# Kernel tuning notes

Hardware: AMD Instinct MI355X
Metric: run time of the kernel (lower is better)

The kernel has to match this reference:

```python
import jax, jax.numpy as jnp
import numpy as np

B, L, N, C = 16, 96, 1024, 3
EMB, GRAP, OUT, NLAYER = 64, 16, 12, 2


def setup_inputs() -> dict:
    key = jax.random.key(0)
    ks = jax.random.split(key, 16)
    s = 0.1
    return {
        "history_data": jax.random.normal(ks[0], (B, L, N, C), jnp.float32),
        # row-stochastic graph (normalized adjacency buffer)
        "adj": jax.nn.softmax(jax.random.normal(ks[1], (N, N), jnp.float32), axis=-1),
        "Wv0": jax.random.normal(ks[2], (C, EMB), jnp.float32) * s,
        "Wv1": jax.random.normal(ks[3], (EMB, EMB), jnp.float32) * s,
        "bv": jnp.zeros((NLAYER, EMB), jnp.float32),
        "E": jax.random.normal(ks[4], (NLAYER, N, EMB), jnp.float32) * s,
        "Wq": jax.random.normal(ks[5], (NLAYER, EMB, EMB), jnp.float32) * s,
        "Wk": jax.random.normal(ks[6], (NLAYER, EMB, EMB), jnp.float32) * s,
        "Eg1": jax.random.normal(ks[7], (NLAYER, N, GRAP), jnp.float32) * s,
        "Eg2": jax.random.normal(ks[8], (NLAYER, N, GRAP), jnp.float32) * s,
        "Wmix": jax.random.normal(ks[9], (NLAYER, 3, EMB, EMB), jnp.float32) * s,
        "bmix": jnp.zeros((NLAYER, EMB), jnp.float32),
        "Wgates": jax.random.normal(ks[10], (NLAYER, 4, EMB, EMB), jnp.float32) * s,
        "bgates": jnp.zeros((NLAYER, 4, EMB), jnp.float32),
        "Wdec": jax.random.normal(ks[11], (OUT, NLAYER, EMB), jnp.float32) * s,
        "bdec": jnp.zeros((OUT,), jnp.float32),
        "Wout": jax.random.normal(ks[12], (OUT, OUT), jnp.float32) * s,
        "bout": jnp.zeros((OUT,), jnp.float32),
    }


def reference(history_data, adj, Wv0, Wv1, bv, E, Wq, Wk, Eg1, Eg2,
              Wmix, bmix, Wgates, bgates, Wdec, bdec, Wout, bout):
    # GinAR forward (inference: dropout = identity, lay_norm unused in original forward).
    emb = Wv1.shape[0]
    inv = 1.0 / jnp.sqrt(jnp.float32(emb))
    x = history_data  # (B, L, N, in)
    finals = []
    for z in range(Wmix.shape[0]):
        Wv = Wv0 if z == 0 else Wv1
        # interpolation attention over variables (nodes), shared across time/batch
        q = E[z] @ Wq[z]
        k = E[z] @ Wk[z]
        attn = jax.nn.softmax((q @ k.T) * inv, axis=-1)                 # (N, N)
        # adaptive learned graph
        adp = jax.nn.softmax(jax.nn.relu(Eg1[z] @ Eg2[z].T), axis=-1)    # (N, N)
        bz, Wm, bm, Wg, bgz = bv[z], Wmix[z], bmix[z], Wgates[z], bgates[z]

        def step(ct, xt, Wv=Wv, attn=attn, adp=adp, bz=bz, Wm=Wm, bm=bm, Wg=Wg, bgz=bgz):
            v = xt @ Wv + bz                                # (B, N, emb)
            h = jnp.einsum('mn,bne->bme', attn, v)          # variable interpolation
            hg = (jnp.einsum('mn,bne->bme', adj, h) @ Wm[0]
                  + jnp.einsum('mn,bne->bme', adp, h) @ Wm[1]
                  + h @ Wm[2] + bm)                         # adaptive graph conv
            gates = jnp.einsum('bne,kef->kbnf', hg, Wg) + bgz[:, None, None, :]
            f = jax.nn.sigmoid(gates[0])
            i = jax.nn.sigmoid(gates[1])
            g = jnp.tanh(gates[2])
            o = jax.nn.sigmoid(gates[3])
            ct = f * ct + i * g
            ht = o * jnp.tanh(ct)
            return ct, ht

        ct0 = jnp.zeros((x.shape[0], x.shape[2], emb), x.dtype)
        _, hts = jax.lax.scan(step, ct0, jnp.moveaxis(x, 1, 0))  # (L, B, N, emb)
        x = jnp.moveaxis(hts, 0, 1)                              # (B, L, N, emb)
        finals.append(x[:, -1])                                  # last step -> (B, N, emb)
    final = jnp.stack(finals, axis=1)                            # (B, layers, N, emb)
    # decoder Conv2d(layer_num -> out_len, kernel (1, emb)) == contraction over (layer, emb)
    dec = jnp.einsum('blne,ole->bon', final, Wdec) + bdec[None, :, None]
    # 1x1 output conv
    out = jnp.einsum('bpn,op->bon', dec, Wout) + bout[None, :, None]
    return out  # (B, out_len, N)
```

## Files before the change

kernel.cpp:

```cpp
#include <hip/hip_runtime.h>
#include <hip/hip_bf16.h>

#define B_ 16
#define L_ 96
#define N_ 1024
#define EMB_ 64

typedef __hip_bfloat16 bf16;
typedef __attribute__((ext_vector_type(4))) float f32x4;
typedef __attribute__((ext_vector_type(8))) short s16x8;

__global__ __launch_bounds__(256) void gemm_nn(
    const float* __restrict__ A, const float* __restrict__ Bm, float* __restrict__ C,
    int M, int N, int K, int lda, int ldb, int ldc, const float* __restrict__ bias)
{
    __shared__ float As[64][17];
    __shared__ __align__(16) float Bs[16][64];
    const int tid = threadIdx.x;
    const int tx = tid & 15, ty = tid >> 4;
    const int row0 = blockIdx.y * 64, col0 = blockIdx.x * 64;
    float acc[4][4] = {};
    const int ak = tid & 15, ar = tid >> 4;
    const int bc = tid & 63, bk = tid >> 6;
    for (int k0 = 0; k0 < K; k0 += 16) {
#pragma unroll
        for (int i = 0; i < 4; ++i) {
            int r = ar + i * 16;
            int gr = row0 + r, gk = k0 + ak;
            As[r][ak] = (gr < M && gk < K) ? A[(size_t)gr * lda + gk] : 0.f;
        }
#pragma unroll
        for (int i = 0; i < 4; ++i) {
            int kk = bk + i * 4;
            int gk = k0 + kk, gc = col0 + bc;
            Bs[kk][bc] = (gk < K && gc < N) ? Bm[(size_t)gk * ldb + gc] : 0.f;
        }
        __syncthreads();
#pragma unroll
        for (int kk = 0; kk < 16; ++kk) {
            float4 b4 = *reinterpret_cast<const float4*>(&Bs[kk][tx * 4]);
            float a0 = As[ty * 4 + 0][kk];
            float a1 = As[ty * 4 + 1][kk];
            float a2 = As[ty * 4 + 2][kk];
            float a3 = As[ty * 4 + 3][kk];
            acc[0][0] += a0 * b4.x; acc[0][1] += a0 * b4.y; acc[0][2] += a0 * b4.z; acc[0][3] += a0 * b4.w;
            acc[1][0] += a1 * b4.x; acc[1][1] += a1 * b4.y; acc[1][2] += a1 * b4.z; acc[1][3] += a1 * b4.w;
            acc[2][0] += a2 * b4.x; acc[2][1] += a2 * b4.y; acc[2][2] += a2 * b4.z; acc[2][3] += a2 * b4.w;
            acc[3][0] += a3 * b4.x; acc[3][1] += a3 * b4.y; acc[3][2] += a3 * b4.z; acc[3][3] += a3 * b4.w;
        }
        __syncthreads();
    }
#pragma unroll
    for (int i = 0; i < 4; ++i) {
        int gr = row0 + ty * 4 + i;
        if (gr >= M) continue;
#pragma unroll
        for (int j = 0; j < 4; ++j) {
            int gc = col0 + tx * 4 + j;
            if (gc >= N) continue;
            float v = acc[i][j];
            if (bias) v += bias[gc];
            C[(size_t)gr * ldc + gc] = v;
        }
    }
}

__global__ __launch_bounds__(256) void gemm_nt(
    const float* __restrict__ A, const float* __restrict__ Bm, float* __restrict__ C,
    int N, int K, float alpha)
{
    __shared__ float As[64][65];
    __shared__ float Bs[64][65];
    const int tid = threadIdx.x;
    const int row0 = blockIdx.y * 64, col0 = blockIdx.x * 64;
    for (int idx = tid; idx < 64 * K; idx += 256) {
        int r = idx / K, c = idx % K;
        As[r][c] = A[(size_t)(row0 + r) * K + c];
        Bs[r][c] = Bm[(size_t)(col0 + r) * K + c];
    }
    __syncthreads();
    const int tx = tid & 15, ty = tid >> 4;
    float acc[4][4] = {};
    for (int c = 0; c < K; ++c) {
        float a[4], b[4];
#pragma unroll
        for (int i = 0; i < 4; ++i) a[i] = As[ty * 4 + i][c];
#pragma unroll
        for (int j = 0; j < 4; ++j) b[j] = Bs[tx * 4 + j][c];
#pragma unroll
        for (int i = 0; i < 4; ++i)
#pragma unroll
            for (int j = 0; j < 4; ++j) acc[i][j] += a[i] * b[j];
    }
#pragma unroll
    for (int i = 0; i < 4; ++i)
#pragma unroll
        for (int j = 0; j < 4; ++j)
            C[(size_t)(row0 + ty * 4 + i) * N + col0 + tx * 4 + j] = alpha * acc[i][j];
}

__global__ __launch_bounds__(256) void row_softmax(
    const float* __restrict__ in, float* __restrict__ out32, int os32,
    bf16* __restrict__ out16, int os16, int relu)
{
    const float* rp = in + (size_t)blockIdx.x * N_;
    const int tid = threadIdx.x;
    float v[4];
#pragma unroll
    for (int j = 0; j < 4; ++j) {
        float x = rp[tid + 256 * j];
        if (relu) x = fmaxf(x, 0.f);
        v[j] = x;
    }
    float m = fmaxf(fmaxf(v[0], v[1]), fmaxf(v[2], v[3]));
#pragma unroll
    for (int off = 32; off > 0; off >>= 1) m = fmaxf(m, __shfl_xor(m, off));
    __shared__ float red[4], red2[4];
    int w = tid >> 6;
    if ((tid & 63) == 0) red[w] = m;
    __syncthreads();
    m = fmaxf(fmaxf(red[0], red[1]), fmaxf(red[2], red[3]));
    float s = 0.f;
#pragma unroll
    for (int j = 0; j < 4; ++j) { v[j] = __expf(v[j] - m); s += v[j]; }
#pragma unroll
    for (int off = 32; off > 0; off >>= 1) s += __shfl_xor(s, off);
    if ((tid & 63) == 0) red2[w] = s;
    __syncthreads();
    s = red2[0] + red2[1] + red2[2] + red2[3];
    float inv = 1.f / s;
#pragma unroll
    for (int j = 0; j < 4; ++j) {
        float r = v[j] * inv;
        if (out32) out32[(size_t)blockIdx.x * os32 + tid + 256 * j] = r;
        if (out16) out16[(size_t)blockIdx.x * os16 + tid + 256 * j] = __float2bfloat16(r);
    }
}

__global__ __launch_bounds__(256) void transpose_f2b(
    const float* __restrict__ in, bf16* __restrict__ out)
{
    __shared__ float t[64][65];
    const int cx = blockIdx.x, cy = blockIdx.y;
    const int tid = threadIdx.x;
#pragma unroll
    for (int k = 0; k < 16; ++k) {
        int idx = k * 256 + tid;
        int r = idx >> 6, c = idx & 63;
        t[r][c] = in[(size_t)(cy * 64 + r) * 1024 + cx * 64 + c];
    }
    __syncthreads();
#pragma unroll
    for (int k = 0; k < 16; ++k) {
        int idx = k * 256 + tid;
        int r = idx >> 6, c = idx & 63;
        out[(size_t)(cx * 64 + r) * 1024 + cy * 64 + c] = __float2bfloat16(t[c][r]);
    }
}

__global__ __launch_bounds__(256) void wgct_kernel(const float* __restrict__ Wg,
                                                   bf16* __restrict__ WgcT)
{
    int i = blockIdx.x * 256 + threadIdx.x;
    int g = i >> 12, e = (i >> 6) & 63, f = i & 63;
    WgcT[(((size_t)g * 64 + f) << 6) + e] = __float2bfloat16(Wg[i]);
}

__global__ __launch_bounds__(256) void wvc1t_kernel(const float* __restrict__ Wvc1,
                                                    bf16* __restrict__ WT)
{
    int i = blockIdx.x * 256 + threadIdx.x;
    int row = i >> 6, f = i & 63;
    float v = 0.f;
    if (row < 192) { int kp = row >> 6, e = row & 63; v = Wvc1[kp * 4096 + f * 64 + e]; }
    WT[i] = __float2bfloat16(v);
}

__global__ __launch_bounds__(256) void f2b_kernel(const float* __restrict__ in,
                                                  bf16* __restrict__ out, int n)
{
    int i = blockIdx.x * 256 + threadIdx.x;
    if (i < n) out[i] = __float2bfloat16(in[i]);
}

__global__ __launch_bounds__(256) void bias_kernel(
    const float* __restrict__ bvz, const float* __restrict__ Wmz, const float* __restrict__ bmz,
    const float* __restrict__ Wgz, const float* __restrict__ bgz, float* __restrict__ bgconst)
{
    __shared__ float bconst[64];
    const int tid = threadIdx.x;
    if (tid < 64) {
        float s = bmz[tid];
        for (int kp = 0; kp < 3; ++kp)
            for (int f = 0; f < 64; ++f) s += bvz[f] * Wmz[kp * 4096 + f * 64 + tid];
        bconst[tid] = s;
    }
    __syncthreads();
    int g = tid >> 6, fo = tid & 63;
    float s = bgz[g * 64 + fo];
    for (int e = 0; e < 64; ++e) s += bconst[e] * Wgz[g * 4096 + e * 64 + fo];
    bgconst[tid] = s;
}

__global__ __launch_bounds__(256) void wbig_kernel(
    const float* __restrict__ Wvc0, const float* __restrict__ Wg0, bf16* __restrict__ WbigT)
{
    const int tid = threadIdx.x;
    const int g = tid >> 6, fo = tid & 63;
    float v[9];
#pragma unroll
    for (int q = 0; q < 9; ++q) {
        const int kp = q / 3, c = q % 3;
        float s = 0.f;
        for (int e = 0; e < 64; ++e)
            s += Wvc0[kp * 192 + c * 64 + e] * Wg0[g * 4096 + e * 64 + fo];
        v[q] = s;
    }
#pragma unroll
    for (int i = 0; i < 32; ++i)
        WbigT[(size_t)tid * 32 + i] = __float2bfloat16(i < 9 ? v[i] : 0.f);
}

__global__ __launch_bounds__(256) void xt_build(
    const float* __restrict__ hist, bf16* __restrict__ XT)
{
    __shared__ float xs[3][1024];
    const int lb = blockIdx.x;
    const int l = lb >> 4, b = lb & 15;
    const int tid = threadIdx.x;
    const float* xp = hist + ((size_t)b * L_ + l) * N_ * 3;
    for (int i = tid; i < 3072; i += 256) xs[i % 3][i / 3] = xp[i];
    __syncthreads();
#pragma unroll
    for (int c = 0; c < 3; ++c)
#pragma unroll
        for (int q = 0; q < 4; ++q) {
            int n = q * 256 + tid;
            XT[((size_t)lb * 3 + c) * 1024 + n] = __float2bfloat16(xs[c][n]);
        }
}

__device__ __forceinline__ void gload16(const bf16* g, bf16* l)
{
    __builtin_amdgcn_global_load_lds((const __attribute__((address_space(1))) void*)g,
                                     (__attribute__((address_space(3))) void*)l, 16, 0, 0);
}

template <int OUT_BF16, int REMAP>
__global__ __launch_bounds__(256) void gemm_mfma(
    const bf16* __restrict__ A, const bf16* __restrict__ BT, void* __restrict__ Cp,
    int M, int N, int K, int lda, int ldb, int ldc,
    const float* __restrict__ bias, int Nmask)
{
    __shared__ __align__(16) bf16 As[128 * 64];
    __shared__ __align__(16) bf16 Bs[128 * 64];
    const int tid = threadIdx.x;
    const int lane = tid & 63, w = tid >> 6;
    const int wr = w >> 1, wc = w & 1;
    const int row0 = blockIdx.y * 128, col0 = blockIdx.x * 128;
    if (REMAP == 1) BT += (size_t)blockIdx.z * 64;
    if (REMAP == 2) A += (size_t)blockIdx.z * 1024;
    if (REMAP == 3) {
        const int z3 = blockIdx.z >> 1, wh = blockIdx.z & 1;
        if (wh) A = BT + (size_t)z3 * 1048576;
        BT = (const bf16*)bias + (size_t)z3 * 1048576;
        Cp = (void*)((bf16*)Cp + (size_t)z3 * 3145728 + (size_t)wh * 1024);
        bias = nullptr;
    }

    f32x4 acc[4][4];
#pragma unroll
    for (int i = 0; i < 4; ++i)
#pragma unroll
        for (int j = 0; j < 4; ++j) acc[i][j] = (f32x4){0.f, 0.f, 0.f, 0.f};

    const int srow = w * 32 + (lane >> 3);
    const int scolsw = ((lane & 7) ^ (lane >> 3)) * 8;

    for (int k0 = 0; k0 < K; k0 += 64) {
#pragma unroll
        for (int i = 0; i < 4; ++i) {
            gload16(A + (size_t)(row0 + srow + i * 8) * lda + k0 + scolsw,
                    &As[(w * 32 + i * 8) * 64]);
            gload16(BT + (size_t)(col0 + srow + i * 8) * ldb + k0 + scolsw,
                    &Bs[(w * 32 + i * 8) * 64]);
        }
        __syncthreads();
#pragma unroll
        for (int kk = 0; kk < 64; kk += 32) {
            s16x8 af[4], bfr[4];
            const int ko = (kk + (lane >> 4) * 8) ^ ((lane & 7) << 3);
#pragma unroll
            for (int mi = 0; mi < 4; ++mi)
                af[mi] = *(const s16x8*)&As[(wr * 64 + mi * 16 + (lane & 15)) * 64 + ko];
#pragma unroll
            for (int ni = 0; ni < 4; ++ni)
                bfr[ni] = *(const s16x8*)&Bs[(wc * 64 + ni * 16 + (lane & 15)) * 64 + ko];
#pragma unroll
            for (int mi = 0; mi < 4; ++mi)
#pragma unroll
                for (int ni = 0; ni < 4; ++ni)
                    acc[mi][ni] = __builtin_amdgcn_mfma_f32_16x16x32_bf16(
                        af[mi], bfr[ni], acc[mi][ni], 0, 0, 0);
        }
        __syncthreads();
    }

    if (REMAP == 1) {
        bf16* outb = (bf16*)Cp + (size_t)blockIdx.z * (64 * 3072);
#pragma unroll
        for (int mi = 0; mi < 4; ++mi) {
            const int gr = row0 + wr * 64 + mi * 16 + (lane >> 4) * 4;
#pragma unroll
            for (int ni = 0; ni < 4; ++ni) {
                const int gc = col0 + wc * 64 + ni * 16 + (lane & 15);
#pragma unroll
                for (int j = 0; j < 4; ++j) {
                    const int r = gr + j;
                    if (r >= Nmask) continue;
                    outb[(size_t)(r & 63) * 3072 + (r >> 6) * 1024 + gc] =
                        __float2bfloat16(acc[mi][ni][j]);
                }
            }
        }
        return;
    }
    if (REMAP == 2) {
        bf16* outb = (bf16*)Cp;
        const int kpoff = blockIdx.z * 3;
#pragma unroll
        for (int mi = 0; mi < 4; ++mi) {
            const int gr = row0 + wr * 64 + mi * 16 + (lane >> 4) * 4;
#pragma unroll
            for (int ni = 0; ni < 4; ++ni) {
                const int gc = col0 + wc * 64 + ni * 16 + (lane & 15);
                if (gc >= Nmask) continue;
                const int dstc = (gc / 3) * 32 + kpoff + gc % 3;
#pragma unroll
                for (int j = 0; j < 4; ++j)
                    outb[(size_t)(gr + j) * ldc + dstc] = __float2bfloat16(acc[mi][ni][j]);
            }
        }
        return;
    }

#pragma unroll
    for (int mi = 0; mi < 4; ++mi) {
        const int gr = row0 + wr * 64 + mi * 16 + (lane >> 4) * 4;
#pragma unroll
        for (int ni = 0; ni < 4; ++ni) {
            const int gc = col0 + wc * 64 + ni * 16 + (lane & 15);
            if (gc >= Nmask) continue;
            const float bb = bias ? bias[gc] : 0.f;
#pragma unroll
            for (int j = 0; j < 4; ++j) {
                float v = acc[mi][ni][j] + bb;
                if (OUT_BF16)
                    ((bf16*)Cp)[(size_t)(gr + j) * ldc + gc] = __float2bfloat16(v);
                else
                    ((float*)Cp)[(size_t)(gr + j) * ldc + gc] = v;
            }
        }
    }
}

__global__ __launch_bounds__(512) void gemm_pipe(
    const bf16* __restrict__ A, const bf16* __restrict__ BT, bf16* __restrict__ C,
    int N, int K)
{
    __shared__ __align__(16) bf16 lds[8 * 8192];
    const int tid = threadIdx.x;
    const int lane = tid & 63, w = tid >> 6;
    const int wm = w >> 2, wn = w & 3, bh = wn >> 1;
    const int row0 = blockIdx.y * 256, col0 = blockIdx.x * 256;

    const int strow = tid >> 3;
    const int srck  = ((tid & 7) ^ ((tid >> 3) & 7)) << 3;
    const int e7 = lane & 7, fs = lane >> 4, a15 = lane & 15;

    int aoff0[8], boff0[4];
#pragma unroll
    for (int mi = 0; mi < 8; ++mi)
        aoff0[mi] = (mi * 16 + a15) * 64 + ((fs ^ e7) << 3);
#pragma unroll
    for (int ni = 0; ni < 4; ++ni)
        boff0[ni] = ((wn & 1) * 64 + ni * 16 + a15) * 64 + ((fs ^ e7) << 3);

    auto stage = [&](int mat, int half, int kt) {
        bf16* dst = &lds[(size_t)((((kt & 1) << 1) | mat) * 2 + half) * 8192 + w * 512];
        const bf16* src = (mat ? BT + (size_t)col0 * K : A + (size_t)row0 * K)
                          + (size_t)(half * 128) * K + kt * 64 + srck;
        gload16(src + (size_t)strow * K, dst);
        gload16(src + (size_t)(64 + strow) * K, dst + 4096);
    };

    f32x4 acc[8][4];
#pragma unroll
    for (int i = 0; i < 8; ++i)
#pragma unroll
        for (int j = 0; j < 4; ++j) acc[i][j] = (f32x4){0.f, 0.f, 0.f, 0.f};

    s16x8 b0, b1, b2, b3;

#define MF_(a, mi) { \
    acc[mi][0] = __builtin_amdgcn_mfma_f32_16x16x32_bf16(a, b0, acc[mi][0], 0, 0, 0); \
    acc[mi][1] = __builtin_amdgcn_mfma_f32_16x16x32_bf16(a, b1, acc[mi][1], 0, 0, 0); \
    acc[mi][2] = __builtin_amdgcn_mfma_f32_16x16x32_bf16(a, b2, acc[mi][2], 0, 0, 0); \
    acc[mi][3] = __builtin_amdgcn_mfma_f32_16x16x32_bf16(a, b3, acc[mi][3], 0, 0, 0); }

#define PH_(d, kh, g, DOB, STG) { \
    const bf16* Ab = &lds[((d) * 4 + wm) * 8192]; \
    const bf16* Bb = &lds[((d) * 4 + 2 + bh) * 8192]; \
    if (DOB) { \
        b0 = *(const s16x8*)&Bb[boff0[0] ^ ((kh) * 32)]; \
        b1 = *(const s16x8*)&Bb[boff0[1] ^ ((kh) * 32)]; \
        b2 = *(const s16x8*)&Bb[boff0[2] ^ ((kh) * 32)]; \
        b3 = *(const s16x8*)&Bb[boff0[3] ^ ((kh) * 32)]; \
    } \
    s16x8 a0 = *(const s16x8*)&Ab[aoff0[(g) * 4 + 0] ^ ((kh) * 32)]; \
    s16x8 a1 = *(const s16x8*)&Ab[aoff0[(g) * 4 + 1] ^ ((kh) * 32)]; \
    s16x8 a2 = *(const s16x8*)&Ab[aoff0[(g) * 4 + 2] ^ ((kh) * 32)]; \
    s16x8 a3 = *(const s16x8*)&Ab[aoff0[(g) * 4 + 3] ^ ((kh) * 32)]; \
    STG; \
    __builtin_amdgcn_s_barrier(); \
    asm volatile("s_waitcnt lgkmcnt(0)" ::: "memory"); \
    __builtin_amdgcn_sched_barrier(0); \
    __builtin_amdgcn_s_setprio(1); \
    MF_(a0, (g) * 4 + 0); MF_(a1, (g) * 4 + 1); \
    MF_(a2, (g) * 4 + 2); MF_(a3, (g) * 4 + 3); \
    __builtin_amdgcn_s_setprio(0); \
    __builtin_amdgcn_s_barrier(); }

    const int NT = K >> 6;
    stage(0, 0, 0); stage(0, 1, 0); stage(1, 0, 0); stage(1, 1, 0);
    stage(0, 0, 1);

    for (int i = 0; i < NT / 2; ++i) {
        const int kt = 2 * i;
        asm volatile("s_waitcnt vmcnt(2)" ::: "memory");
        __builtin_amdgcn_sched_barrier(0);
        __builtin_amdgcn_s_barrier();
        PH_(0, 0, 0, 1, { stage(0, 1, kt + 1); });
        PH_(0, 0, 1, 0, { stage(1, 0, kt + 1); });
        PH_(0, 1, 0, 1, { stage(1, 1, kt + 1); });
        PH_(0, 1, 1, 0, { if (kt + 2 < NT) stage(0, 0, kt + 2); });
        if (kt + 2 < NT) { asm volatile("s_waitcnt vmcnt(2)" ::: "memory"); }
        else             { asm volatile("s_waitcnt vmcnt(0)" ::: "memory"); }
        __builtin_amdgcn_sched_barrier(0);
        __builtin_amdgcn_s_barrier();
        PH_(1, 0, 0, 1, { if (kt + 2 < NT) stage(0, 1, kt + 2); });
        PH_(1, 0, 1, 0, { if (kt + 2 < NT) stage(1, 0, kt + 2); });
        PH_(1, 1, 0, 1, { if (kt + 2 < NT) stage(1, 1, kt + 2); });
        PH_(1, 1, 1, 0, { if (kt + 3 < NT) stage(0, 0, kt + 3); });
    }
#undef PH_
#undef MF_

#pragma unroll
    for (int mi = 0; mi < 8; ++mi) {
        const int gr = row0 + wm * 128 + mi * 16 + (lane >> 4) * 4;
#pragma unroll
        for (int ni = 0; ni < 4; ++ni) {
            const int gc = col0 + wn * 64 + ni * 16 + (lane & 15);
#pragma unroll
            for (int j = 0; j < 4; ++j)
                C[(size_t)(gr + j) * N + gc] = __float2bfloat16(acc[mi][ni][j]);
        }
    }
}

__global__ __launch_bounds__(256, 4) void fused_gates_scan(
    const bf16* __restrict__ HG, const bf16* __restrict__ WgcT,
    const float* __restrict__ bgc, float* __restrict__ ct_buf,
    bf16* __restrict__ ht_out, float* __restrict__ htlast,
    int LC, int l0, int initct)
{
    __shared__ __align__(16) bf16 Bs[256 * 64];
    __shared__ float bgs[256];
    const int tid = threadIdx.x;
    const int lane = tid & 63, w = tid >> 6;
    const int n = blockIdx.x;
    const int swz = ((lane & 7) ^ (lane >> 3)) * 8;
    const int l8 = (lane >> 3) * 64;

#pragma unroll
    for (int r = 0; r < 8; ++r)
        gload16(WgcT + r * 2048 + w * 512 + l8 + swz, &Bs[r * 2048 + w * 512]);
    bgs[tid] = bgc[tid];
    __syncthreads();

    const int ar = lane & 15;
    const int ak = (lane >> 4) * 8;
    const int kswz = (lane & 7) << 3;
    const int f = w * 16 + ar;
    const int r0 = (lane >> 4) * 4;
    const float bgf = bgs[f], bgi = bgs[64 + f], bgg = bgs[128 + f], bgo = bgs[192 + f];

    float ct[4];
    const size_t cbase = (size_t)n * 1024;
#pragma unroll
    for (int j = 0; j < 4; ++j)
        ct[j] = initct ? 0.f : ct_buf[cbase + (size_t)(r0 + j) * 64 + f];

    const bf16* HGn = HG + (size_t)n * LC * 1024;
    s16x8 a0 = *(const s16x8*)&HGn[ar * 64 + ak];
    s16x8 a1 = *(const s16x8*)&HGn[ar * 64 + ak + 32];

    for (int l = 0; l < LC; ++l) {
        s16x8 p0 = a0, p1 = a1;
        if (l + 1 < LC) {
            p0 = *(const s16x8*)&HGn[((l + 1) * 16 + ar) * 64 + ak];
            p1 = *(const s16x8*)&HGn[((l + 1) * 16 + ar) * 64 + ak + 32];
        }
        f32x4 acc[4];
#pragma unroll
        for (int ni = 0; ni < 4; ++ni) acc[ni] = (f32x4){0.f, 0.f, 0.f, 0.f};
#pragma unroll
        for (int ni = 0; ni < 4; ++ni) {
            s16x8 bf = *(const s16x8*)&Bs[(ni * 64 + w * 16 + ar) * 64 + (ak ^ kswz)];
            acc[ni] = __builtin_amdgcn_mfma_f32_16x16x32_bf16(a0, bf, acc[ni], 0, 0, 0);
        }
#pragma unroll
        for (int ni = 0; ni < 4; ++ni) {
            s16x8 bf = *(const s16x8*)&Bs[(ni * 64 + w * 16 + ar) * 64 + ((ak + 32) ^ kswz)];
            acc[ni] = __builtin_amdgcn_mfma_f32_16x16x32_bf16(a1, bf, acc[ni], 0, 0, 0);
        }
        const size_t hbase = ((size_t)n * LC + l) * 1024;
        const bool last = (l0 + l == L_ - 1);
#pragma unroll
        for (int j = 0; j < 4; ++j) {
            float xf = acc[0][j] + bgf;
            float xi = acc[1][j] + bgi;
            float xg = acc[2][j] + bgg;
            float xo = acc[3][j] + bgo;
            float fg = 1.f / (1.f + __expf(-xf));
            float ig = 1.f / (1.f + __expf(-xi));
            float gg = 2.f / (1.f + __expf(-2.f * xg)) - 1.f;
            float og = 1.f / (1.f + __expf(-xo));
            ct[j] = fg * ct[j] + ig * gg;
            float ht = og * (2.f / (1.f + __expf(-2.f * ct[j])) - 1.f);
            if (ht_out) ht_out[hbase + (size_t)(r0 + j) * 64 + f] = __float2bfloat16(ht);
            if (htlast && last) htlast[cbase + (size_t)(r0 + j) * 64 + f] = ht;
        }
        a0 = p0; a1 = p1;
    }
#pragma unroll
    for (int j = 0; j < 4; ++j)
        ct_buf[cbase + (size_t)(r0 + j) * 64 + f] = ct[j];
}

__global__ __launch_bounds__(256, 4) void fused_gates_scan_y(
    const bf16* __restrict__ Y, const bf16* __restrict__ WbigT,
    const float* __restrict__ bgc, float* __restrict__ ct_buf,
    bf16* __restrict__ ht_out, float* __restrict__ htlast,
    int LC, int l0, int initct)
{
    __shared__ bf16 Bs2[256 * 40];
    __shared__ float bgs[256];
    const int tid = threadIdx.x;
    const int lane = tid & 63, w = tid >> 6;
    const int n = blockIdx.x;
    {
        const uint4* src = (const uint4*)(WbigT + (size_t)tid * 32);
        uint4* dst = (uint4*)&Bs2[tid * 40];
        dst[0] = src[0]; dst[1] = src[1]; dst[2] = src[2]; dst[3] = src[3];
    }
    bgs[tid] = bgc[tid];
    __syncthreads();

    const int ar = lane & 15, fs = lane >> 4;
    const int f = w * 16 + ar;
    const int r0 = fs * 4;
    const float bgf = bgs[f], bgi = bgs[64 + f], bgg = bgs[128 + f], bgo = bgs[192 + f];

    float ct[4];
    const size_t cbase = (size_t)n * 1024;
#pragma unroll
    for (int j = 0; j < 4; ++j)
        ct[j] = initct ? 0.f : ct_buf[cbase + (size_t)(r0 + j) * 64 + f];

    const bf16* Yn = Y + (size_t)n * LC * 512;
    s16x8 a = *(const s16x8*)&Yn[ar * 32 + fs * 8];

    for (int l = 0; l < LC; ++l) {
        s16x8 p = a;
        if (l + 1 < LC) p = *(const s16x8*)&Yn[((l + 1) * 16 + ar) * 32 + fs * 8];
        f32x4 acc[4];
#pragma unroll
        for (int ni = 0; ni < 4; ++ni) {
            s16x8 bf = *(const s16x8*)&Bs2[(ni * 64 + w * 16 + ar) * 40 + fs * 8];
            acc[ni] = __builtin_amdgcn_mfma_f32_16x16x32_bf16(
                a, bf, (f32x4){0.f, 0.f, 0.f, 0.f}, 0, 0, 0);
        }
        const size_t hbase = ((size_t)n * LC + l) * 1024;
        const bool last = (l0 + l == L_ - 1);
#pragma unroll
        for (int j = 0; j < 4; ++j) {
            float xf = acc[0][j] + bgf;
            float xi = acc[1][j] + bgi;
            float xg = acc[2][j] + bgg;
            float xo = acc[3][j] + bgo;
            float fg = 1.f / (1.f + __expf(-xf));
            float ig = 1.f / (1.f + __expf(-xi));
            float gg = 2.f / (1.f + __expf(-2.f * xg)) - 1.f;
            float og = 1.f / (1.f + __expf(-xo));
            ct[j] = fg * ct[j] + ig * gg;
            float ht = og * (2.f / (1.f + __expf(-2.f * ct[j])) - 1.f);
            if (ht_out) ht_out[hbase + (size_t)(r0 + j) * 64 + f] = __float2bfloat16(ht);
            if (htlast && last) htlast[cbase + (size_t)(r0 + j) * 64 + f] = ht;
        }
        a = p;
    }
#pragma unroll
    for (int j = 0; j < 4; ++j)
        ct_buf[cbase + (size_t)(r0 + j) * 64 + f] = ct[j];
}

__global__ __launch_bounds__(256) void decoder_kernel(
    const float* __restrict__ h0, const float* __restrict__ h1,
    const float* __restrict__ Wdec, const float* __restrict__ bdec,
    const float* __restrict__ Wout, const float* __restrict__ bout,
    float* __restrict__ outp)
{
    __shared__ float Wd[12 * 2 * 64];
    __shared__ float Wo[144];
    __shared__ float bd[12], bo[12];
    const int tid = threadIdx.x;
    for (int i = tid; i < 12 * 2 * 64; i += 256) Wd[i] = Wdec[i];
    for (int i = tid; i < 144; i += 256) Wo[i] = Wout[i];
    if (tid < 12) { bd[tid] = bdec[tid]; bo[tid] = bout[tid]; }
    __syncthreads();
    const int gid = blockIdx.x * 256 + tid;
    const int b = gid >> 10, n = gid & 1023;
    const float* h0r = h0 + ((size_t)n * 16 + b) * 64;
    const float* h1r = h1 + ((size_t)n * 16 + b) * 64;
    float dec[12];
#pragma unroll
    for (int o = 0; o < 12; ++o) dec[o] = bd[o];
    for (int e = 0; e < 64; ++e) {
        float v0 = h0r[e], v1 = h1r[e];
#pragma unroll
        for (int o = 0; o < 12; ++o) dec[o] += v0 * Wd[o * 128 + e] + v1 * Wd[o * 128 + 64 + e];
    }
#pragma unroll
    for (int o = 0; o < 12; ++o) {
        float s = bo[o];
#pragma unroll
        for (int p = 0; p < 12; ++p) s += Wo[o * 12 + p] * dec[p];
        outp[((size_t)b * 12 + o) * 1024 + n] = s;
    }
}

extern "C" void kernel_launch(void* const* d_in, const int* in_sizes, int n_in,
                              void* d_out, int out_size, void* d_ws, size_t ws_size,
                              hipStream_t stream)
{
    const float* hist = (const float*)d_in[0];
    const float* adj  = (const float*)d_in[1];
    const float* Wv0  = (const float*)d_in[2];
    const float* Wv1  = (const float*)d_in[3];
    const float* bv   = (const float*)d_in[4];
    const float* E    = (const float*)d_in[5];
    const float* Wq   = (const float*)d_in[6];
    const float* Wk   = (const float*)d_in[7];
    const float* Eg1  = (const float*)d_in[8];
    const float* Eg2  = (const float*)d_in[9];
    const float* Wmix = (const float*)d_in[10];
    const float* bmix = (const float*)d_in[11];
    const float* Wg   = (const float*)d_in[12];
    const float* bg   = (const float*)d_in[13];
    const float* Wdec = (const float*)d_in[14];
    const float* bdec = (const float*)d_in[15];
    const float* Wout = (const float*)d_in[16];
    const float* bout = (const float*)d_in[17];
    float* outp = (float*)d_out;
    (void)in_sizes; (void)n_in; (void)out_size;

    char* ws = (char*)d_ws;
    size_t off = 0;
    auto alloc = [&](size_t bytes) -> void* {
        void* p = (void*)(ws + off);
        off += (bytes + 255) & ~(size_t)255;
        return p;
    };
    bf16*  Mcatb  = (bf16*)alloc((size_t)2 * 1024 * 3072 * 2);
    bf16*  attnT2 = (bf16*)alloc((size_t)2 * 1024 * 1024 * 2);
    bf16*  adjb   = (bf16*)alloc((size_t)1024 * 1024 * 2);
    bf16*  adpb2  = (bf16*)alloc((size_t)2 * 1024 * 1024 * 2);
    float* qb     = (float*)alloc((size_t)1024 * 64 * 4);
    float* kb     = (float*)alloc((size_t)1024 * 64 * 4);
    float* logits = (float*)alloc((size_t)1024 * 1024 * 4);
    float* Wvc0   = (float*)alloc(3 * 3 * 64 * 4);
    float* Wvc1   = (float*)alloc(3 * 64 * 64 * 4);
    bf16*  Wvc1T  = (bf16*)alloc(256 * 64 * 2);
    bf16*  WgcT1  = (bf16*)alloc(256 * 64 * 2);
    bf16*  WbigT  = (bf16*)alloc(256 * 32 * 2);
    float* bgc0   = (float*)alloc(256 * 4);
    float* bgc1   = (float*)alloc(256 * 4);
    float* ct0    = (float*)alloc((size_t)N_ * B_ * 64 * 4);
    float* ct1    = (float*)alloc((size_t)N_ * B_ * 64 * 4);
    float* hl0    = (float*)alloc((size_t)N_ * B_ * 64 * 4);
    float* hl1    = (float*)alloc((size_t)N_ * B_ * 64 * 4);
    bf16*  XT     = (bf16*)alloc((size_t)L_ * 16 * 3 * 1024 * 2);
    size_t fixed = off;

    static const int divs[] = {16, 8};
    int LC = 8;
    for (int di = 0; di < 2; ++di) {
        if (fixed + (size_t)divs[di] * 9437184ull + 65536 <= ws_size) { LC = divs[di]; break; }
    }
    bf16*  VcatT = (bf16*)alloc((size_t)LC * 6291456ull);
    bf16*  HGht  = (bf16*)alloc((size_t)LC * 2097152ull);
    bf16*  Y     = (bf16*)alloc((size_t)LC * 1048576ull);

    dim3 blk(256);
    bf16*  McatB[2] = {Mcatb, Mcatb + 3145728};
    float* bgc[2] = {bgc0, bgc1};

    f2b_kernel<<<4096, blk, 0, stream>>>(adj, adjb, 1024 * 1024);
    for (int z = 0; z < 2; ++z) {
        const float* Ez = E + (size_t)z * N_ * 64;
        gemm_nn<<<dim3(1, 16), blk, 0, stream>>>(Ez, Wq + z * 4096, qb, 1024, 64, 64, 64, 64, 64, nullptr);
        gemm_nn<<<dim3(1, 16), blk, 0, stream>>>(Ez, Wk + z * 4096, kb, 1024, 64, 64, 64, 64, 64, nullptr);
        gemm_nt<<<dim3(16, 16), blk, 0, stream>>>(qb, kb, logits, 1024, 64, 0.125f);
        row_softmax<<<1024, blk, 0, stream>>>(logits, logits, 1024, McatB[z] + 2048, 3072, 0);
        transpose_f2b<<<dim3(16, 16), blk, 0, stream>>>(logits, attnT2 + (size_t)z * 1048576);
        gemm_nt<<<dim3(16, 16), blk, 0, stream>>>(Eg1 + z * 16384, Eg2 + z * 16384, logits, 1024, 16, 1.f);
        row_softmax<<<1024, blk, 0, stream>>>(logits, nullptr, 0, adpb2 + (size_t)z * 1048576, 1024, 1);
        if (z == 0) {
            for (int kp = 0; kp < 3; ++kp)
                gemm_nn<<<dim3(1, 1), blk, 0, stream>>>(Wv0, Wmix + kp * 4096,
                    Wvc0 + kp * 3 * 64, 3, 64, 64, 64, 64, 64, nullptr);
            wbig_kernel<<<1, blk, 0, stream>>>(Wvc0, Wg, WbigT);
        } else {
            for (int kp = 0; kp < 3; ++kp)
                gemm_nn<<<dim3(1, 1), blk, 0, stream>>>(Wv1, Wmix + 12288 + kp * 4096,
                    Wvc1 + kp * 4096, 64, 64, 64, 64, 64, 64, nullptr);
            wvc1t_kernel<<<64, blk, 0, stream>>>(Wvc1, Wvc1T);
            wgct_kernel<<<64, blk, 0, stream>>>(Wg + 16384, WgcT1);
        }
        bias_kernel<<<1, blk, 0, stream>>>(bv + z * 64, Wmix + z * 12288, bmix + z * 64,
            Wg + z * 16384, bg + z * 256, bgc[z]);
    }
    gemm_mfma<1, 3><<<dim3(8, 8, 4), blk, 0, stream>>>(adjb, adpb2, Mcatb,
        1024, 1024, 1024, 1024, 1024, 3072, (const float*)attnT2, 1024);

    hipMemsetAsync(Y, 0, (size_t)LC * 1048576ull, stream);
    xt_build<<<L_ * 16, blk, 0, stream>>>(hist, XT);

    const int nch = L_ / LC;
    dim3 blk512(512);
    for (int c = 0; c < nch; ++c) {
        const int l0 = c * LC;
        gemm_mfma<1, 2><<<dim3(LC * 48 / 128, 8, 3), blk, 0, stream>>>(McatB[0],
            XT + (size_t)l0 * 49152, Y,
            1024, LC * 48, 1024, 3072, 1024, LC * 512, nullptr, LC * 48);
        fused_gates_scan_y<<<1024, blk, 0, stream>>>(Y, WbigT, bgc0, ct0,
            HGht, hl0, LC, l0, c == 0);
        gemm_mfma<1, 1><<<dim3(8, 2, LC * 16), blk, 0, stream>>>(Wvc1T, HGht, VcatT,
            256, 1024, 64, 64, LC * 1024, 0, nullptr, 192);
        gemm_pipe<<<dim3(LC * 4, 4), blk512, 0, stream>>>(McatB[1], VcatT, HGht,
            LC * 1024, 3072);
        fused_gates_scan<<<1024, blk, 0, stream>>>(HGht, WgcT1, bgc1, ct1,
            nullptr, hl1, LC, l0, c == 0);
    }
    decoder_kernel<<<64, blk, 0, stream>>>(hl0, hl1, Wdec, bdec, Wout, bout, outp);
}
```

Measured before the change: 1.632 ms.

## Restructure bf16 GEMM pipeline to 4-stage K=32 ring with packed-row LDS layout

The 256x256 bf16 MFMA GEMM moves from a double-buffered K=64 tile schedule with eight phases per iteration to a four-slot ring of K=32 tiles with three tiles prefetched ahead. The LDS layout packs two matrix rows per 64-element line with a new XOR swizzle, and each wave now reads its own 128-row A and 64-column B slices. The aim is deeper prefetch and fewer barriers per unit of MFMA work, hiding global-load latency better. The trade-off is smaller K steps, which means more loop iterations and more vmcnt/barrier synchronization per K, plus the risk of LDS bank conflicts under the new swizzle.

```diff
diff --git a/kernel.cpp b/kernel.cpp
--- a/kernel.cpp
+++ b/kernel.cpp
@@ -371,28 +371,48 @@
     __shared__ __align__(16) bf16 lds[8 * 8192];
     const int tid = threadIdx.x;
     const int lane = tid & 63, w = tid >> 6;
-    const int wm = w >> 2, wn = w & 3, bh = wn >> 1;
+    const int wm = w >> 2, wn = w & 3;
     const int row0 = blockIdx.y * 256, col0 = blockIdx.x * 256;
 
-    const int strow = tid >> 3;
-    const int srck  = ((tid & 7) ^ ((tid >> 3) & 7)) << 3;
-    const int e7 = lane & 7, fs = lane >> 4, a15 = lane & 15;
-
-    int aoff0[8], boff0[4];
-#pragma unroll
-    for (int mi = 0; mi < 8; ++mi)
-        aoff0[mi] = (mi * 16 + a15) * 64 + ((fs ^ e7) << 3);
-#pragma unroll
-    for (int ni = 0; ni < 4; ++ni)
-        boff0[ni] = ((wn & 1) * 64 + ni * 16 + a15) * 64 + ((fs ^ e7) << 3);
-
-    auto stage = [&](int mat, int half, int kt) {
-        bf16* dst = &lds[(size_t)((((kt & 1) << 1) | mat) * 2 + half) * 8192 + w * 512];
-        const bf16* src = (mat ? BT + (size_t)col0 * K : A + (size_t)row0 * K)
-                          + (size_t)(half * 128) * K + kt * 64 + srck;
-        gload16(src + (size_t)strow * K, dst);
-        gload16(src + (size_t)(64 + strow) * K, dst + 4096);
+    int sm[2], sk[2], sl[2];
+#pragma unroll
+    for (int c = 0; c < 2; ++c) {
+        int g = (c * 8 + w) * 64 + lane;
+        int l = g >> 3, rem = g & 7;
+        int h = rem >> 2, sx = rem & 3;
+        sm[c] = 2 * l + h;
+        sk[c] = (sx ^ (l & 3)) * 8;
+        sl[c] = (c * 8 + w) * 512;
+    }
+    int aoff[8], boff[4];
+    const int fs = lane >> 4;
+#pragma unroll
+    for (int mi = 0; mi < 8; ++mi) {
+        int m = wm * 128 + mi * 16 + (lane & 15);
+        aoff[mi] = (m >> 1) * 64 + (m & 1) * 32 + ((fs ^ ((m >> 1) & 3)) * 8);
+    }
+#pragma unroll
+    for (int ni = 0; ni < 4; ++ni) {
+        int n = wn * 64 + ni * 16 + (lane & 15);
+        boff[ni] = (n >> 1) * 64 + (n & 1) * 32 + ((fs ^ ((n >> 1) & 3)) * 8);
+    }
+
+    const bf16* Abase = A + (size_t)row0 * K;
+    const bf16* Bbase = BT + (size_t)col0 * K;
+    auto stageA = [&](int t) {
+        bf16* dst = &lds[(size_t)((t & 3) * 2) * 8192];
+        const bf16* src = Abase + t * 32;
+#pragma unroll
+        for (int c = 0; c < 2; ++c)
+            gload16(src + (size_t)sm[c] * K + sk[c], dst + sl[c]);
     };
+    auto stageB = [&](int t) {
+        bf16* dst = &lds[(size_t)((t & 3) * 2 + 1) * 8192];
+        const bf16* src = Bbase + t * 32;
+#pragma unroll
+        for (int c = 0; c < 2; ++c)
+            gload16(src + (size_t)sm[c] * K + sk[c], dst + sl[c]);
+    };
 
     f32x4 acc[8][4];
 #pragma unroll
@@ -400,61 +420,52 @@
 #pragma unroll
         for (int j = 0; j < 4; ++j) acc[i][j] = (f32x4){0.f, 0.f, 0.f, 0.f};
 
-    s16x8 b0, b1, b2, b3;
-
-#define MF_(a, mi) { \
-    acc[mi][0] = __builtin_amdgcn_mfma_f32_16x16x32_bf16(a, b0, acc[mi][0], 0, 0, 0); \
-    acc[mi][1] = __builtin_amdgcn_mfma_f32_16x16x32_bf16(a, b1, acc[mi][1], 0, 0, 0); \
-    acc[mi][2] = __builtin_amdgcn_mfma_f32_16x16x32_bf16(a, b2, acc[mi][2], 0, 0, 0); \
-    acc[mi][3] = __builtin_amdgcn_mfma_f32_16x16x32_bf16(a, b3, acc[mi][3], 0, 0, 0); }
-
-#define PH_(d, kh, g, DOB, STG) { \
-    const bf16* Ab = &lds[((d) * 4 + wm) * 8192]; \
-    const bf16* Bb = &lds[((d) * 4 + 2 + bh) * 8192]; \
-    if (DOB) { \
-        b0 = *(const s16x8*)&Bb[boff0[0] ^ ((kh) * 32)]; \
-        b1 = *(const s16x8*)&Bb[boff0[1] ^ ((kh) * 32)]; \
-        b2 = *(const s16x8*)&Bb[boff0[2] ^ ((kh) * 32)]; \
-        b3 = *(const s16x8*)&Bb[boff0[3] ^ ((kh) * 32)]; \
-    } \
-    s16x8 a0 = *(const s16x8*)&Ab[aoff0[(g) * 4 + 0] ^ ((kh) * 32)]; \
-    s16x8 a1 = *(const s16x8*)&Ab[aoff0[(g) * 4 + 1] ^ ((kh) * 32)]; \
-    s16x8 a2 = *(const s16x8*)&Ab[aoff0[(g) * 4 + 2] ^ ((kh) * 32)]; \
-    s16x8 a3 = *(const s16x8*)&Ab[aoff0[(g) * 4 + 3] ^ ((kh) * 32)]; \
-    STG; \
-    __builtin_amdgcn_s_barrier(); \
-    asm volatile("s_waitcnt lgkmcnt(0)" ::: "memory"); \
-    __builtin_amdgcn_sched_barrier(0); \
-    __builtin_amdgcn_s_setprio(1); \
-    MF_(a0, (g) * 4 + 0); MF_(a1, (g) * 4 + 1); \
-    MF_(a2, (g) * 4 + 2); MF_(a3, (g) * 4 + 3); \
-    __builtin_amdgcn_s_setprio(0); \
-    __builtin_amdgcn_s_barrier(); }
-
-    const int NT = K >> 6;
-    stage(0, 0, 0); stage(0, 1, 0); stage(1, 0, 0); stage(1, 1, 0);
-    stage(0, 0, 1);
-
-    for (int i = 0; i < NT / 2; ++i) {
-        const int kt = 2 * i;
-        asm volatile("s_waitcnt vmcnt(2)" ::: "memory");
+#define MFG(ai, areg) { \
+    acc[ai][0] = __builtin_amdgcn_mfma_f32_16x16x32_bf16(areg, b0, acc[ai][0], 0, 0, 0); \
+    acc[ai][1] = __builtin_amdgcn_mfma_f32_16x16x32_bf16(areg, b1, acc[ai][1], 0, 0, 0); \
+    acc[ai][2] = __builtin_amdgcn_mfma_f32_16x16x32_bf16(areg, b2, acc[ai][2], 0, 0, 0); \
+    acc[ai][3] = __builtin_amdgcn_mfma_f32_16x16x32_bf16(areg, b3, acc[ai][3], 0, 0, 0); }
+
+    const int NT = K >> 5;
+    stageB(0); stageA(0); stageB(1); stageA(1); stageB(2); stageA(2);
+
+    for (int t = 0; t < NT; ++t) {
+        const bf16* Ab = &lds[(size_t)((t & 3) * 2) * 8192];
+        const bf16* Bb = Ab + 8192;
+        if (t + 2 < NT)      { asm volatile("s_waitcnt vmcnt(8)" ::: "memory"); }
+        else if (t + 1 < NT) { asm volatile("s_waitcnt vmcnt(4)" ::: "memory"); }
+        else                 { asm volatile("s_waitcnt vmcnt(0)" ::: "memory"); }
         __builtin_amdgcn_sched_barrier(0);
         __builtin_amdgcn_s_barrier();
-        PH_(0, 0, 0, 1, { stage(0, 1, kt + 1); });
-        PH_(0, 0, 1, 0, { stage(1, 0, kt + 1); });
-        PH_(0, 1, 0, 1, { stage(1, 1, kt + 1); });
-        PH_(0, 1, 1, 0, { if (kt + 2 < NT) stage(0, 0, kt + 2); });
-        if (kt + 2 < NT) { asm volatile("s_waitcnt vmcnt(2)" ::: "memory"); }
-        else             { asm volatile("s_waitcnt vmcnt(0)" ::: "memory"); }
+        s16x8 b0 = *(const s16x8*)&Bb[boff[0]];
+        s16x8 b1 = *(const s16x8*)&Bb[boff[1]];
+        s16x8 b2 = *(const s16x8*)&Bb[boff[2]];
+        s16x8 b3 = *(const s16x8*)&Bb[boff[3]];
+        s16x8 a0 = *(const s16x8*)&Ab[aoff[0]];
+        s16x8 a1 = *(const s16x8*)&Ab[aoff[1]];
+        s16x8 a2 = *(const s16x8*)&Ab[aoff[2]];
+        s16x8 a3 = *(const s16x8*)&Ab[aoff[3]];
+        if (t + 3 < NT) stageB(t + 3);
+        __builtin_amdgcn_s_barrier();
+        asm volatile("s_waitcnt lgkmcnt(0)" ::: "memory");
         __builtin_amdgcn_sched_barrier(0);
+        __builtin_amdgcn_s_setprio(1);
+        MFG(0, a0) MFG(1, a1) MFG(2, a2) MFG(3, a3)
+        __builtin_amdgcn_s_setprio(0);
         __builtin_amdgcn_s_barrier();
-        PH_(1, 0, 0, 1, { if (kt + 2 < NT) stage(0, 1, kt + 2); });
-        PH_(1, 0, 1, 0, { if (kt + 2 < NT) stage(1, 0, kt + 2); });
-        PH_(1, 1, 0, 1, { if (kt + 2 < NT) stage(1, 1, kt + 2); });
-        PH_(1, 1, 1, 0, { if (kt + 3 < NT) stage(0, 0, kt + 3); });
-    }
-#undef PH_
-#undef MF_
+        s16x8 a4 = *(const s16x8*)&Ab[aoff[4]];
+        s16x8 a5 = *(const s16x8*)&Ab[aoff[5]];
+        s16x8 a6 = *(const s16x8*)&Ab[aoff[6]];
+        s16x8 a7 = *(const s16x8*)&Ab[aoff[7]];
+        if (t + 3 < NT) stageA(t + 3);
+        __builtin_amdgcn_s_barrier();
+        asm volatile("s_waitcnt lgkmcnt(0)" ::: "memory");
+        __builtin_amdgcn_sched_barrier(0);
+        __builtin_amdgcn_s_setprio(1);
+        MFG(4, a4) MFG(5, a5) MFG(6, a6) MFG(7, a7)
+        __builtin_amdgcn_s_setprio(0);
+    }
+#undef MFG
 
 #pragma unroll
     for (int mi = 0; mi < 8; ++mi) {
```

After: 1.643 ms. About the same (+0.7%).
